# Kernel optimization log

Measured on AMD Instinct MI355X. Metric: run time of the kernel, lower is better.

## Reference

```python
import jax, jax.numpy as jnp
import numpy as np

EPS = 1e-5

def lrelu(x):
    return jnp.where(x >= 0, x, 0.1 * x)

def bn_eval(x, g, b, m, v):
    # eval-mode BatchNorm over the last (channel) axis
    return (x - m) * (g * jax.lax.rsqrt(v + EPS)) + b

def setup_inputs():
    key = jax.random.key(0)
    ks = jax.random.split(key, 12)
    Nq, K, Cin, Fc, Co = 20000, 32, 3, 64, 64
    q_points = jax.random.normal(ks[0], (Nq, Cin), jnp.float32)
    s_points = jax.random.normal(ks[1], (Nq, Cin), jnp.float32)
    feat = jax.random.normal(ks[2], (Nq, Fc), jnp.float32)
    # valid indices 0..Nq (Nq == shadow/pad row appended in forward)
    neighb_inds = jax.random.randint(ks[3], (Nq, K), 0, Nq + 1)
    def w(k, shape, fan_in):
        return jax.random.normal(k, shape, jnp.float32) / np.float32(np.sqrt(fan_in))
    W_pos2 = w(ks[4], (Fc, Cin), Cin)          # convpos2: Conv2d(Cin, Fc, 1)
    W_attn = w(ks[5], (Co * Cin, Fc), Fc)      # convattn: Conv2d(Fc, Co*Cin, 1)
    W_res = w(ks[6], (Co, Fc), Fc)             # residual 1x1 conv
    def bn(k, c):
        k1, k2, k3, k4 = jax.random.split(k, 4)
        return (jax.random.normal(k1, (c,), jnp.float32) * 0.1 + 1.0,
                jax.random.normal(k2, (c,), jnp.float32) * 0.1,
                jax.random.normal(k3, (c,), jnp.float32) * 0.1,
                jax.random.uniform(k4, (c,), jnp.float32) * 0.5 + 0.5)
    bq = bn(ks[7], Fc); bp = bn(ks[8], Cin); b1 = bn(ks[9], Co); br = bn(ks[10], Co)
    return dict(q_points=q_points, s_points=s_points, neighb_inds=neighb_inds, feat=feat,
                W_pos2=W_pos2, W_attn=W_attn, W_res=W_res,
                bnq_g=bq[0], bnq_b=bq[1], bnq_m=bq[2], bnq_v=bq[3],
                bnp_g=bp[0], bnp_b=bp[1], bnp_m=bp[2], bnp_v=bp[3],
                bn1_g=b1[0], bn1_b=b1[1], bn1_m=b1[2], bn1_v=b1[3],
                bnr_g=br[0], bnr_b=br[1], bnr_m=br[2], bnr_v=br[3])

def reference(q_points, s_points, neighb_inds, feat, W_pos2, W_attn, W_res,
              bnq_g, bnq_b, bnq_m, bnq_v, bnp_g, bnp_b, bnp_m, bnp_v,
              bn1_g, bn1_b, bn1_m, bn1_v, bnr_g, bnr_b, bnr_m, bnr_v):
    Nq, Cin = q_points.shape
    Fc = feat.shape[1]
    Co = W_res.shape[0]
    K = neighb_inds.shape[1]
    # append shadow (zero) row for out-of-range neighbor indices
    s_pad = jnp.concatenate([s_points, jnp.zeros((1, Cin), s_points.dtype)], 0)
    f_pad = jnp.concatenate([feat, jnp.zeros((1, Fc), feat.dtype)], 0)
    xg = s_pad[neighb_inds]                      # [Nq,K,Cin] EFR_P gather
    yg = f_pad[neighb_inds]                      # [Nq,K,Fc]  EFR_F gather
    x_v = xg - q_points[:, None, :]              # [Nq,K,Cin] values
    x_q = lrelu(bn_eval(feat, bnq_g, bnq_b, bnq_m, bnq_v))          # [Nq,Fc]
    pos0 = lrelu(bn_eval(s_points, bnp_g, bnp_b, bnp_m, bnp_v))     # [Nq,Cin]
    pos = (pos0[:, None, :] - x_v) @ W_pos2.T                       # [Nq,K,Fc]
    attn = x_q[:, None, :] - yg + pos                               # [Nq,K,Fc]
    attn = jax.nn.softmax(attn / jnp.sqrt(jnp.float32(Fc)), axis=1) # softmax over K
    attn = (attn @ W_attn.T).reshape(Nq, K, Co, Cin)                # [Nq,K,Co,Cin]
    y_e = jnp.einsum('nkoi,nki->nko', attn, x_v)                    # [Nq,K,Co]
    y_e = lrelu(bn_eval(y_e, bn1_g, bn1_b, bn1_m, bn1_v))
    res = bn_eval(yg @ W_res.T, bnr_g, bnr_b, bnr_m, bnr_v)         # [Nq,K,Co]
    y_e = lrelu(y_e + res)
    return y_e.max(axis=1)                                          # [Nq,Co]
```

## Files before the change

kernel.cpp:

```cpp
#include <hip/hip_runtime.h>
#include <hip/hip_bf16.h>
#include <math.h>

#define KNB 32
#define FC 64
#define CO 64
#define EPS 1e-5f
#define NBLOCKS 1024
#define CL 0.180336880095853f

typedef __attribute__((ext_vector_type(8))) short short8;
typedef __attribute__((ext_vector_type(4))) float floatx4;
typedef __attribute__((ext_vector_type(2))) float float2v;

#if __has_builtin(__builtin_amdgcn_exp2f)
#define EXP2F(x) __builtin_amdgcn_exp2f(x)
#else
#define EXP2F(x) exp2f(x)
#endif
#if __has_builtin(__builtin_amdgcn_rcpf)
#define RCPF(x) __builtin_amdgcn_rcpf(x)
#else
#define RCPF(x) (1.f / (x))
#endif

__device__ __forceinline__ unsigned pk2(float a, float b) {
    __hip_bfloat162 h = __float22bfloat162_rn(float2{a, b});
    unsigned u; __builtin_memcpy(&u, &h, 4); return u;
}
__device__ __forceinline__ unsigned pk2v(float2v v) { return pk2(v.x, v.y); }
__device__ __forceinline__ float lrelu(float x) { return fmaxf(x, 0.1f * x); }
__device__ __forceinline__ float2v fma2(float2v a, float2v b, float2v c) {
    return __builtin_elementwise_fma(a, b, c);
}
__device__ __forceinline__ float2v lrelu2(float2v x) {
    return __builtin_elementwise_max(x, 0.1f * x);
}

__global__ __launch_bounds__(256, 4) void GCT_61272003445298_kernel(
    const float* __restrict__ q_points,
    const float* __restrict__ s_points,
    const int*   __restrict__ neighb,
    const float* __restrict__ feat,
    const float* __restrict__ W_pos2,
    const float* __restrict__ W_attn,
    const float* __restrict__ W_res,
    const float* __restrict__ bnq_g, const float* __restrict__ bnq_b,
    const float* __restrict__ bnq_m, const float* __restrict__ bnq_v,
    const float* __restrict__ bnp_g, const float* __restrict__ bnp_b,
    const float* __restrict__ bnp_m, const float* __restrict__ bnp_v,
    const float* __restrict__ bn1_g, const float* __restrict__ bn1_b,
    const float* __restrict__ bn1_m, const float* __restrict__ bn1_v,
    const float* __restrict__ bnr_g, const float* __restrict__ bnr_b,
    const float* __restrict__ bnr_m, const float* __restrict__ bnr_v,
    float* __restrict__ out, int Nq)
{
    const int t = threadIdx.x;
    const int wv = t >> 6;
    const int lane = t & 63;
    const int cc = lane & 15, quad = lane >> 4;
    const int o = wv * 16 + cc;
    const int qB  = t >> 7;
    const int kg  = lane >> 3;
    const int fqB = (((t >> 6) & 1) << 3) + (lane & 7);

    __shared__ __align__(16) short sA1[64 * 72];
    __shared__ __align__(16) short sA2[64 * 72];
    __shared__ float sXv[64][4];
    __shared__ __align__(16) float sWp2[192];
    __shared__ __align__(16) float sQs[64], sQb[64];

    if (t < 192) sWp2[t] = CL * W_pos2[t];
    if (t < 64) {
        float sc = bnq_g[t] * rsqrtf(bnq_v[t] + EPS);
        sQs[t] = sc; sQb[t] = bnq_b[t] - bnq_m[t] * sc;
    }
    const float ps0 = bnp_g[0] * rsqrtf(bnp_v[0] + EPS);
    const float ps1 = bnp_g[1] * rsqrtf(bnp_v[1] + EPS);
    const float ps2 = bnp_g[2] * rsqrtf(bnp_v[2] + EPS);
    const float pb0 = bnp_b[0] - bnp_m[0] * ps0;
    const float pb1 = bnp_b[1] - bnp_m[1] * ps1;
    const float pb2 = bnp_b[2] - bnp_m[2] * ps2;
    const float e1s = bn1_g[o] * rsqrtf(bn1_v[o] + EPS);
    const float e1b = bn1_b[o] - bn1_m[o] * e1s;
    const float ers = bnr_g[o] * rsqrtf(bnr_v[o] + EPS);
    const float erb = bnr_b[o] - bnr_m[o] * ers;

    short8 bW[4][2];
    #pragma unroll
    for (int ty = 0; ty < 4; ++ty) {
        const float* wrow = (ty < 3) ? (W_attn + (long)(o * 3 + ty) * FC)
                                     : (W_res  + (long)o * FC);
        const float sc = (ty < 3) ? e1s : ers;
        #pragma unroll
        for (int ks = 0; ks < 2; ++ks) {
            int k0 = ks * 32 + quad * 8;
            float4 w0 = *(const float4*)(wrow + k0);
            float4 w1 = *(const float4*)(wrow + k0 + 4);
            uint4 pv;
            pv.x = pk2(w0.x * sc, w0.y * sc);
            pv.y = pk2(w0.z * sc, w0.w * sc);
            pv.z = pk2(w1.x * sc, w1.y * sc);
            pv.w = pk2(w1.z * sc, w1.w * sc);
            __builtin_memcpy(&bW[ty][ks], &pv, 16);
        }
    }
    __syncthreads();

    float2v wpa[3], wpb[3];
    {
        const float* w = &sWp2[fqB * 12];
        wpa[0] = (float2v){w[0], w[3]};  wpa[1] = (float2v){w[1], w[4]};
        wpa[2] = (float2v){w[2], w[5]};
        wpb[0] = (float2v){w[6], w[9]};  wpb[1] = (float2v){w[7], w[10]};
        wpb[2] = (float2v){w[8], w[11]};
    }
    const float4 qs4 = *(const float4*)&sQs[fqB * 4];
    const float4 qb4 = *(const float4*)&sQb[fqB * 4];
    const float4* __restrict__ feat4 = (const float4*)feat;

    const int npair = (Nq + 1) >> 1;
    for (int p = blockIdx.x; p < npair; p += NBLOCKS) {
        const long n0 = 2L * p;
        long n1 = n0 + 1;
        const bool has1 = (n1 < Nq);
        if (!has1) n1 = n0;
        const long nn = qB ? n1 : n0;

        const float nq0 = -q_points[nn * 3 + 0];
        const float nq1 = -q_points[nn * 3 + 1];
        const float nq2 = -q_points[nn * 3 + 2];
        const float pp0 = lrelu(fmaf(s_points[nn * 3 + 0], ps0, pb0));
        const float pp1 = lrelu(fmaf(s_points[nn * 3 + 1], ps1, pb1));
        const float pp2 = lrelu(fmaf(s_points[nn * 3 + 2], ps2, pb2));
        const int4 idx4 = *(const int4*)(neighb + nn * KNB + kg * 4);

        float2v xqcA, xqcB;
        {
            const float4 fx = feat4[(int)(nn * 16) + fqB];
            float2v xqA = lrelu2(fma2((float2v){fx.x, fx.y},
                                      (float2v){qs4.x, qs4.y},
                                      (float2v){qb4.x, qb4.y}));
            float2v xqB = lrelu2(fma2((float2v){fx.z, fx.w},
                                      (float2v){qs4.z, qs4.w},
                                      (float2v){qb4.z, qb4.w}));
            const float2v v0 = (float2v){pp0, pp0};
            const float2v v1 = (float2v){pp1, pp1};
            const float2v v2 = (float2v){pp2, pp2};
            xqcA = fma2(v0, wpa[0], fma2(v1, wpa[1], fma2(v2, wpa[2], CL * xqA)));
            xqcB = fma2(v0, wpb[0], fma2(v1, wpb[1], fma2(v2, wpb[2], CL * xqB)));
        }

        short* a1b = &sA1[(qB * 32 + kg * 4) * 72 + fqB * 4];
        short* a2b = &sA2[(qB * 32 + kg * 4) * 72 + fqB * 4];
        float2v evA[4], evB[4];
        float2v sumA = (float2v){0.f, 0.f}, sumB = (float2v){0.f, 0.f};
        #pragma unroll
        for (int j = 0; j < 4; ++j) {
            const int idx = ((const int*)&idx4)[j];
            const float sel = (idx < Nq) ? 1.f : 0.f;
            const int idc = (idx < Nq) ? idx : 0;
            float4 y = feat4[idc * 16 + fqB];
            y.x *= sel; y.y *= sel; y.z *= sel; y.w *= sel;
            uint2 pk; pk.x = pk2(y.x, y.y); pk.y = pk2(y.z, y.w);
            *(uint2*)(a2b + j * 72) = pk;
            const float xv0 = fmaf(s_points[idc * 3 + 0], sel, nq0);
            const float xv1 = fmaf(s_points[idc * 3 + 1], sel, nq1);
            const float xv2 = fmaf(s_points[idc * 3 + 2], sel, nq2);
            if (fqB == 0) {
                float4 xvv = {xv0, xv1, xv2, 0.f};
                *(float4*)&sXv[qB * 32 + kg * 4 + j][0] = xvv;
            }
            const float2v m0 = (float2v){-xv0, -xv0};
            const float2v m1 = (float2v){-xv1, -xv1};
            const float2v m2 = (float2v){-xv2, -xv2};
            float2v lA = fma2((float2v){y.x, y.y}, (float2v){-CL, -CL}, xqcA);
            lA = fma2(m0, wpa[0], lA); lA = fma2(m1, wpa[1], lA); lA = fma2(m2, wpa[2], lA);
            float2v lB = fma2((float2v){y.z, y.w}, (float2v){-CL, -CL}, xqcB);
            lB = fma2(m0, wpb[0], lB); lB = fma2(m1, wpb[1], lB); lB = fma2(m2, wpb[2], lB);
            evA[j] = (float2v){EXP2F(lA.x), EXP2F(lA.y)};
            evB[j] = (float2v){EXP2F(lB.x), EXP2F(lB.y)};
            sumA = sumA + evA[j];
            sumB = sumB + evB[j];
        }
        float s0 = sumA.x, s1 = sumA.y, s2 = sumB.x, s3 = sumB.y;
        s0 += __shfl_xor(s0, 8); s0 += __shfl_xor(s0, 16); s0 += __shfl_xor(s0, 32);
        s1 += __shfl_xor(s1, 8); s1 += __shfl_xor(s1, 16); s1 += __shfl_xor(s1, 32);
        s2 += __shfl_xor(s2, 8); s2 += __shfl_xor(s2, 16); s2 += __shfl_xor(s2, 32);
        s3 += __shfl_xor(s3, 8); s3 += __shfl_xor(s3, 16); s3 += __shfl_xor(s3, 32);
        const float2v invA = (float2v){RCPF(s0), RCPF(s1)};
        const float2v invB = (float2v){RCPF(s2), RCPF(s3)};
        #pragma unroll
        for (int j = 0; j < 4; ++j) {
            uint2 pw;
            pw.x = pk2v(evA[j] * invA);
            pw.y = pk2v(evB[j] * invB);
            *(uint2*)(a1b + j * 72) = pw;
        }
        __syncthreads();

        float m0r = -1e30f, m1r = -1e30f;
        #pragma unroll
        for (int mt = 0; mt < 4; ++mt) {
            floatx4 acc[4];
            #pragma unroll
            for (int ty = 0; ty < 4; ++ty) acc[ty] = (floatx4){0.f, 0.f, 0.f, 0.f};
            const int r0 = mt * 16 + cc;
            #pragma unroll
            for (int ks = 0; ks < 2; ++ks) {
                const int kof = ks * 32 + quad * 8;
                short8 a1 = *(const short8*)(sA1 + r0 * 72 + kof);
                short8 a2 = *(const short8*)(sA2 + r0 * 72 + kof);
                acc[0] = __builtin_amdgcn_mfma_f32_16x16x32_bf16(a1, bW[0][ks], acc[0], 0, 0, 0);
                acc[1] = __builtin_amdgcn_mfma_f32_16x16x32_bf16(a1, bW[1][ks], acc[1], 0, 0, 0);
                acc[2] = __builtin_amdgcn_mfma_f32_16x16x32_bf16(a1, bW[2][ks], acc[2], 0, 0, 0);
                acc[3] = __builtin_amdgcn_mfma_f32_16x16x32_bf16(a2, bW[3][ks], acc[3], 0, 0, 0);
            }
            #pragma unroll
            for (int reg = 0; reg < 4; ++reg) {
                const int r = mt * 16 + quad * 4 + reg;
                float4 xv = *(const float4*)&sXv[r][0];
                float y = acc[0][reg] * xv.x + acc[1][reg] * xv.y + acc[2][reg] * xv.z;
                float v = lrelu(y + e1b) + acc[3][reg];
                if (mt < 2) m0r = fmaxf(m0r, v); else m1r = fmaxf(m1r, v);
            }
        }
        m0r = fmaxf(m0r, __shfl_xor(m0r, 16));
        m0r = fmaxf(m0r, __shfl_xor(m0r, 32));
        m1r = fmaxf(m1r, __shfl_xor(m1r, 16));
        m1r = fmaxf(m1r, __shfl_xor(m1r, 32));
        if (lane < 16) {
            out[n0 * CO + o] = lrelu(m0r + erb);
            if (has1) out[n1 * CO + o] = lrelu(m1r + erb);
        }
        __syncthreads();
    }
}

extern "C" void kernel_launch(void* const* d_in, const int* in_sizes, int n_in,
                              void* d_out, int out_size, void* d_ws, size_t ws_size,
                              hipStream_t stream) {
    const float* q_points = (const float*)d_in[0];
    const float* s_points = (const float*)d_in[1];
    const int*   neighb   = (const int*)  d_in[2];
    const float* feat     = (const float*)d_in[3];
    const float* W_pos2   = (const float*)d_in[4];
    const float* W_attn   = (const float*)d_in[5];
    const float* W_res    = (const float*)d_in[6];
    const float* bnq_g = (const float*)d_in[7];
    const float* bnq_b = (const float*)d_in[8];
    const float* bnq_m = (const float*)d_in[9];
    const float* bnq_v = (const float*)d_in[10];
    const float* bnp_g = (const float*)d_in[11];
    const float* bnp_b = (const float*)d_in[12];
    const float* bnp_m = (const float*)d_in[13];
    const float* bnp_v = (const float*)d_in[14];
    const float* bn1_g = (const float*)d_in[15];
    const float* bn1_b = (const float*)d_in[16];
    const float* bn1_m = (const float*)d_in[17];
    const float* bn1_v = (const float*)d_in[18];
    const float* bnr_g = (const float*)d_in[19];
    const float* bnr_b = (const float*)d_in[20];
    const float* bnr_m = (const float*)d_in[21];
    const float* bnr_v = (const float*)d_in[22];
    float* out = (float*)d_out;

    int Nq = in_sizes[0] / 3;

    hipLaunchKernelGGL(GCT_61272003445298_kernel,
                       dim3(NBLOCKS), dim3(256), 0, stream,
                       q_points, s_points, neighb, feat, W_pos2, W_attn, W_res,
                       bnq_g, bnq_b, bnq_m, bnq_v,
                       bnp_g, bnp_b, bnp_m, bnp_v,
                       bn1_g, bn1_b, bn1_m, bn1_v,
                       bnr_g, bnr_b, bnr_m, bnr_v,
                       out, Nq);
}
```

Before: 160.4 us.

## Software-pipeline neighbor gathers across pair iterations and use lightweight barriers

Moves the gathers of neighbor features and positions for the next point pair into registers so they are issued before the MFMA stage of the current pair, overlapping global-memory latency with compute. Neighbor indices are prefetched two iterations ahead. Invalid neighbors now read from a zeroed workspace buffer instead of being clamped and masked. __syncthreads is replaced with an LDS-only waitcnt plus s_barrier. The cost is higher register pressure from the live prefetched data, plus an extra memset launch that depends on the workspace being present.

```diff
diff --git a/kernel.cpp b/kernel.cpp
--- a/kernel.cpp
+++ b/kernel.cpp
@@ -23,6 +23,8 @@
 #else
 #define RCPF(x) (1.f / (x))
 #endif
+
+#define LGKM_BARRIER() asm volatile("s_waitcnt lgkmcnt(0)\n\ts_barrier" ::: "memory")
 
 __device__ __forceinline__ unsigned pk2(float a, float b) {
     __hip_bfloat162 h = __float22bfloat162_rn(float2{a, b});
@@ -53,11 +55,13 @@
     const float* __restrict__ bn1_m, const float* __restrict__ bn1_v,
     const float* __restrict__ bnr_g, const float* __restrict__ bnr_b,
     const float* __restrict__ bnr_m, const float* __restrict__ bnr_v,
+    const float* __restrict__ zp,
     float* __restrict__ out, int Nq)
 {
     const int t = threadIdx.x;
     const int wv = t >> 6;
     const int lane = t & 63;
+    const int bid = blockIdx.x;
     const int cc = lane & 15, quad = lane >> 4;
     const int o = wv * 16 + cc;
     const int qB  = t >> 7;
@@ -115,90 +119,119 @@
         wpb[0] = (float2v){w[6], w[9]};  wpb[1] = (float2v){w[7], w[10]};
         wpb[2] = (float2v){w[8], w[11]};
     }
-    const float4 qs4 = *(const float4*)&sQs[fqB * 4];
-    const float4 qb4 = *(const float4*)&sQb[fqB * 4];
     const float4* __restrict__ feat4 = (const float4*)feat;
+    short* const a1b = &sA1[(qB * 32 + kg * 4) * 72 + fqB * 4];
+    short* const a2b = &sA2[(qB * 32 + kg * 4) * 72 + fqB * 4];
 
     const int npair = (Nq + 1) >> 1;
-    for (int p = blockIdx.x; p < npair; p += NBLOCKS) {
+
+    float4 gF[4];
+    float  xv0v[4], xv1v[4], xv2v[4];
+    float2v xqcA, xqcB;
+    int4 idxN;
+
+    auto prep = [&](int4 idx4, int pr) {
+        const long nn = 2L * pr + qB;
+        const float q0 = q_points[nn * 3 + 0];
+        const float q1 = q_points[nn * 3 + 1];
+        const float q2 = q_points[nn * 3 + 2];
+        const float so0 = s_points[nn * 3 + 0];
+        const float so1 = s_points[nn * 3 + 1];
+        const float so2 = s_points[nn * 3 + 2];
+        const float4 fx = feat4[(int)(nn * 16) + fqB];
+        #pragma unroll
+        for (int j = 0; j < 4; ++j) {
+            const int idx = ((const int*)&idx4)[j];
+            const bool valid = (idx < Nq);
+            const float* fb = valid ? (feat + (long)idx * FC) : zp;
+            const float* sb = valid ? (s_points + (long)idx * 3) : zp;
+            gF[j] = *(const float4*)(fb + fqB * 4);
+            xv0v[j] = sb[0] - q0;
+            xv1v[j] = sb[1] - q1;
+            xv2v[j] = sb[2] - q2;
+        }
+        const float pp0 = lrelu(fmaf(so0, ps0, pb0));
+        const float pp1 = lrelu(fmaf(so1, ps1, pb1));
+        const float pp2 = lrelu(fmaf(so2, ps2, pb2));
+        const float4 qs4 = *(const float4*)&sQs[fqB * 4];
+        const float4 qb4 = *(const float4*)&sQb[fqB * 4];
+        float2v xqA = lrelu2(fma2((float2v){fx.x, fx.y},
+                                  (float2v){qs4.x, qs4.y},
+                                  (float2v){qb4.x, qb4.y}));
+        float2v xqB = lrelu2(fma2((float2v){fx.z, fx.w},
+                                  (float2v){qs4.z, qs4.w},
+                                  (float2v){qb4.z, qb4.w}));
+        const float2v v0 = (float2v){pp0, pp0};
+        const float2v v1 = (float2v){pp1, pp1};
+        const float2v v2 = (float2v){pp2, pp2};
+        xqcA = fma2(v0, wpa[0], fma2(v1, wpa[1], fma2(v2, wpa[2], CL * xqA)));
+        xqcB = fma2(v0, wpb[0], fma2(v1, wpb[1], fma2(v2, wpb[2], CL * xqB)));
+    };
+
+    {
+        int4 i0 = *(const int4*)(neighb + (2L * bid + qB) * KNB + kg * 4);
+        prep(i0, bid);
+        const int pn = bid + NBLOCKS;
+        const int pcl = (pn < npair) ? pn : bid;
+        idxN = *(const int4*)(neighb + (2L * pcl + qB) * KNB + kg * 4);
+    }
+
+    for (int p = bid; p < npair; p += NBLOCKS) {
+        {
+            float2v evA[4], evB[4];
+            float2v sumA = (float2v){0.f, 0.f}, sumB = (float2v){0.f, 0.f};
+            #pragma unroll
+            for (int j = 0; j < 4; ++j) {
+                const float4 y = gF[j];
+                uint2 pk; pk.x = pk2(y.x, y.y); pk.y = pk2(y.z, y.w);
+                *(uint2*)(a2b + j * 72) = pk;
+                const float xv0 = xv0v[j], xv1 = xv1v[j], xv2 = xv2v[j];
+                if (fqB == 0) {
+                    float4 xvv = {xv0, xv1, xv2, 0.f};
+                    *(float4*)&sXv[qB * 32 + kg * 4 + j][0] = xvv;
+                }
+                const float2v m0 = (float2v){-xv0, -xv0};
+                const float2v m1 = (float2v){-xv1, -xv1};
+                const float2v m2 = (float2v){-xv2, -xv2};
+                float2v lA = fma2((float2v){y.x, y.y}, (float2v){-CL, -CL}, xqcA);
+                lA = fma2(m0, wpa[0], lA); lA = fma2(m1, wpa[1], lA); lA = fma2(m2, wpa[2], lA);
+                float2v lB = fma2((float2v){y.z, y.w}, (float2v){-CL, -CL}, xqcB);
+                lB = fma2(m0, wpb[0], lB); lB = fma2(m1, wpb[1], lB); lB = fma2(m2, wpb[2], lB);
+                evA[j] = (float2v){EXP2F(lA.x), EXP2F(lA.y)};
+                evB[j] = (float2v){EXP2F(lB.x), EXP2F(lB.y)};
+                sumA = sumA + evA[j];
+                sumB = sumB + evB[j];
+            }
+            float s0 = sumA.x, s1 = sumA.y, s2 = sumB.x, s3 = sumB.y;
+            s0 += __shfl_xor(s0, 8); s0 += __shfl_xor(s0, 16); s0 += __shfl_xor(s0, 32);
+            s1 += __shfl_xor(s1, 8); s1 += __shfl_xor(s1, 16); s1 += __shfl_xor(s1, 32);
+            s2 += __shfl_xor(s2, 8); s2 += __shfl_xor(s2, 16); s2 += __shfl_xor(s2, 32);
+            s3 += __shfl_xor(s3, 8); s3 += __shfl_xor(s3, 16); s3 += __shfl_xor(s3, 32);
+            const float2v invA = (float2v){RCPF(s0), RCPF(s1)};
+            const float2v invB = (float2v){RCPF(s2), RCPF(s3)};
+            #pragma unroll
+            for (int j = 0; j < 4; ++j) {
+                uint2 pw;
+                pw.x = pk2v(evA[j] * invA);
+                pw.y = pk2v(evB[j] * invB);
+                *(uint2*)(a1b + j * 72) = pw;
+            }
+        }
+        LGKM_BARRIER();
+
+        const int pn = p + NBLOCKS;
+        if (pn < npair) {
+            int4 icur = idxN;
+            const int pnn = pn + NBLOCKS;
+            const int pcl = (pnn < npair) ? pnn : pn;
+            idxN = *(const int4*)(neighb + (2L * pcl + qB) * KNB + kg * 4);
+            prep(icur, pn);
+        }
+
         const long n0 = 2L * p;
         long n1 = n0 + 1;
         const bool has1 = (n1 < Nq);
         if (!has1) n1 = n0;
-        const long nn = qB ? n1 : n0;
-
-        const float nq0 = -q_points[nn * 3 + 0];
-        const float nq1 = -q_points[nn * 3 + 1];
-        const float nq2 = -q_points[nn * 3 + 2];
-        const float pp0 = lrelu(fmaf(s_points[nn * 3 + 0], ps0, pb0));
-        const float pp1 = lrelu(fmaf(s_points[nn * 3 + 1], ps1, pb1));
-        const float pp2 = lrelu(fmaf(s_points[nn * 3 + 2], ps2, pb2));
-        const int4 idx4 = *(const int4*)(neighb + nn * KNB + kg * 4);
-
-        float2v xqcA, xqcB;
-        {
-            const float4 fx = feat4[(int)(nn * 16) + fqB];
-            float2v xqA = lrelu2(fma2((float2v){fx.x, fx.y},
-                                      (float2v){qs4.x, qs4.y},
-                                      (float2v){qb4.x, qb4.y}));
-            float2v xqB = lrelu2(fma2((float2v){fx.z, fx.w},
-                                      (float2v){qs4.z, qs4.w},
-                                      (float2v){qb4.z, qb4.w}));
-            const float2v v0 = (float2v){pp0, pp0};
-            const float2v v1 = (float2v){pp1, pp1};
-            const float2v v2 = (float2v){pp2, pp2};
-            xqcA = fma2(v0, wpa[0], fma2(v1, wpa[1], fma2(v2, wpa[2], CL * xqA)));
-            xqcB = fma2(v0, wpb[0], fma2(v1, wpb[1], fma2(v2, wpb[2], CL * xqB)));
-        }
-
-        short* a1b = &sA1[(qB * 32 + kg * 4) * 72 + fqB * 4];
-        short* a2b = &sA2[(qB * 32 + kg * 4) * 72 + fqB * 4];
-        float2v evA[4], evB[4];
-        float2v sumA = (float2v){0.f, 0.f}, sumB = (float2v){0.f, 0.f};
-        #pragma unroll
-        for (int j = 0; j < 4; ++j) {
-            const int idx = ((const int*)&idx4)[j];
-            const float sel = (idx < Nq) ? 1.f : 0.f;
-            const int idc = (idx < Nq) ? idx : 0;
-            float4 y = feat4[idc * 16 + fqB];
-            y.x *= sel; y.y *= sel; y.z *= sel; y.w *= sel;
-            uint2 pk; pk.x = pk2(y.x, y.y); pk.y = pk2(y.z, y.w);
-            *(uint2*)(a2b + j * 72) = pk;
-            const float xv0 = fmaf(s_points[idc * 3 + 0], sel, nq0);
-            const float xv1 = fmaf(s_points[idc * 3 + 1], sel, nq1);
-            const float xv2 = fmaf(s_points[idc * 3 + 2], sel, nq2);
-            if (fqB == 0) {
-                float4 xvv = {xv0, xv1, xv2, 0.f};
-                *(float4*)&sXv[qB * 32 + kg * 4 + j][0] = xvv;
-            }
-            const float2v m0 = (float2v){-xv0, -xv0};
-            const float2v m1 = (float2v){-xv1, -xv1};
-            const float2v m2 = (float2v){-xv2, -xv2};
-            float2v lA = fma2((float2v){y.x, y.y}, (float2v){-CL, -CL}, xqcA);
-            lA = fma2(m0, wpa[0], lA); lA = fma2(m1, wpa[1], lA); lA = fma2(m2, wpa[2], lA);
-            float2v lB = fma2((float2v){y.z, y.w}, (float2v){-CL, -CL}, xqcB);
-            lB = fma2(m0, wpb[0], lB); lB = fma2(m1, wpb[1], lB); lB = fma2(m2, wpb[2], lB);
-            evA[j] = (float2v){EXP2F(lA.x), EXP2F(lA.y)};
-            evB[j] = (float2v){EXP2F(lB.x), EXP2F(lB.y)};
-            sumA = sumA + evA[j];
-            sumB = sumB + evB[j];
-        }
-        float s0 = sumA.x, s1 = sumA.y, s2 = sumB.x, s3 = sumB.y;
-        s0 += __shfl_xor(s0, 8); s0 += __shfl_xor(s0, 16); s0 += __shfl_xor(s0, 32);
-        s1 += __shfl_xor(s1, 8); s1 += __shfl_xor(s1, 16); s1 += __shfl_xor(s1, 32);
-        s2 += __shfl_xor(s2, 8); s2 += __shfl_xor(s2, 16); s2 += __shfl_xor(s2, 32);
-        s3 += __shfl_xor(s3, 8); s3 += __shfl_xor(s3, 16); s3 += __shfl_xor(s3, 32);
-        const float2v invA = (float2v){RCPF(s0), RCPF(s1)};
-        const float2v invB = (float2v){RCPF(s2), RCPF(s3)};
-        #pragma unroll
-        for (int j = 0; j < 4; ++j) {
-            uint2 pw;
-            pw.x = pk2v(evA[j] * invA);
-            pw.y = pk2v(evB[j] * invB);
-            *(uint2*)(a1b + j * 72) = pw;
-        }
-        __syncthreads();
-
         float m0r = -1e30f, m1r = -1e30f;
         #pragma unroll
         for (int mt = 0; mt < 4; ++mt) {
@@ -233,7 +266,7 @@
             out[n0 * CO + o] = lrelu(m0r + erb);
             if (has1) out[n1 * CO + o] = lrelu(m1r + erb);
         }
-        __syncthreads();
+        LGKM_BARRIER();
     }
 }
 
@@ -267,6 +300,9 @@
 
     int Nq = in_sizes[0] / 3;
 
+    size_t zn = ws_size < 4096 ? ws_size : (size_t)4096;
+    hipMemsetAsync(d_ws, 0, zn, stream);
+
     hipLaunchKernelGGL(GCT_61272003445298_kernel,
                        dim3(NBLOCKS), dim3(256), 0, stream,
                        q_points, s_points, neighb, feat, W_pos2, W_attn, W_res,
@@ -274,5 +310,5 @@
                        bnp_g, bnp_b, bnp_m, bnp_v,
                        bn1_g, bn1_b, bn1_m, bn1_v,
                        bnr_g, bnr_b, bnr_m, bnr_v,
-                       out, Nq);
-}
+                       (const float*)d_ws, out, Nq);
+}
```

Result: slower. 199.5 us (+24.3%).
